# Performance work log

Measured on AMD Instinct MI355X. Metric: run time of the kernel, lower is better.

Reference implementation:

```python
import jax, jax.numpy as jnp
import numpy as np
import math

# Config (matches init_kwargs / input_specs)
N_ENT = 50000      # number of entities
N_REL = 500        # number of relations
HID = 64           # args.hidden_dim = per-axis dim d; entity dim = 3d, relation dim = 4d
E = 500000         # number of edges
EMB_RANGE = 1.0    # embedding_range
PI = 3.1415926235897933


def setup_inputs() -> dict:
    key = jax.random.key(0)
    k1, k2, k3, k4, k5 = jax.random.split(key, 5)
    entities = jax.random.normal(k1, (N_ENT, 3 * HID), dtype=jnp.float32)
    relations = jax.random.normal(k2, (N_REL, 4 * HID), dtype=jnp.float32)
    head = jax.random.randint(k3, (E,), 0, N_ENT, dtype=jnp.int32)
    rel = jax.random.randint(k4, (E,), 0, N_REL, dtype=jnp.int32)
    tail = jax.random.randint(k5, (E,), 0, N_ENT, dtype=jnp.int32)
    edge_index = jnp.stack([head, rel, tail], axis=0)  # (3, E)
    return {"entities": entities, "relations": relations, "edge_index": edge_index}


def do_trans(ent, rel):
    """Rot3DE rotation: rotate 3D entity point (per feature dim) by the
    quaternion encoded in rel = (axis_x, axis_y, axis_z, theta). is_head_rel=True branch.
    ent: (E, 3d), rel: (E, 4d) -> (E, 4d)"""
    ex, ey, ez = jnp.split(ent, 3, axis=-1)            # each (E, d)
    rx, ry, rz, theta = jnp.split(rel, 4, axis=-1)     # each (E, d)
    theta = theta / (EMB_RANGE / PI)
    sin = jnp.sin(theta)
    w = jnp.cos(theta)
    # F.normalize(stack([sin*rx, sin*ry, sin*rz]), dim=0): unit rotation axis (sign of sin folded in)
    t = jnp.stack([sin * rx, sin * ry, sin * rz], axis=0)  # (3, E, d)
    norm = jnp.sqrt(jnp.sum(t * t, axis=0, keepdims=True))
    n = t / jnp.maximum(norm, 1e-12)
    # quaternion q = (w, u) with u = |sin(theta)| * unit_axis  (sin sign already in n)
    s = jnp.sqrt(jnp.clip(1.0 - w * w, 0.0, None))
    ux, uy, uz = s * n[0], s * n[1], s * n[2]
    # Hamilton product q (x) p with pure quaternion p = (0, ex, ey, ez)  [head direction]
    x_score = w * ex + (uy * ez - uz * ey)
    y_score = w * ey + (uz * ex - ux * ez)
    z_score = w * ez + (ux * ey - uy * ex)
    w_score = -(ux * ex + uy * ey + uz * ez)
    return jnp.concatenate([x_score, y_score, z_score, w_score], axis=-1)  # (E, 4d)


def reference(entities, relations, edge_index):
    head, rel_id, tail = edge_index[0], edge_index[1], edge_index[2]
    # eff_do_trans's unique-based dedup is a pure compute optimization; the
    # math is identical to the direct per-edge transform below.
    qv = do_trans(entities[head], relations[rel_id])  # (E, 4d) keys/values
    # GAT_update: key = [gathered tail entity (3d) ; zeros(d)]
    k = jnp.concatenate(
        [entities[tail], jnp.zeros((E, HID), dtype=entities.dtype)], axis=-1
    )  # (E, 4d)
    embed_dim = 4 * HID
    alpha = jnp.sum(k * qv, axis=-1) / math.sqrt(embed_dim)  # (E,)
    # scatter_softmax over destination nodes (stable segment softmax)
    m = jax.ops.segment_max(alpha, tail, num_segments=N_ENT)
    m = jnp.where(jnp.isfinite(m), m, 0.0)  # empty segments
    e = jnp.exp(alpha - m[tail])
    denom = jax.ops.segment_sum(e, tail, num_segments=N_ENT)
    attn = e / denom[tail]  # (E,)
    # weighted scatter_add -> (N_ENT, 4d)
    out = jax.ops.segment_sum(qv * attn[:, None], tail, num_segments=N_ENT)
    return out
```

## Files before the change

### kernel.cpp

```cpp
#include <hip/hip_runtime.h>
#include <stdint.h>
#include <math.h>

#define HID 64
#define PI_F 3.14159262235897933f

__global__ void prep(const float* __restrict__ rel, float4* __restrict__ quat, int nrel,
                     const int* __restrict__ eidx, int E, int* __restrict__ hist,
                     int qblocks) {
    if ((int)blockIdx.x < qblocks) {
        int i = blockIdx.x * blockDim.x + threadIdx.x;
        if (i >= nrel * HID) return;
        int r = i >> 6, j = i & 63;
        const float* base = rel + (size_t)r * 4 * HID;
        float rx = base[j];
        float ry = base[HID + j];
        float rz = base[2 * HID + j];
        float th = base[3 * HID + j];
        float theta = th * PI_F;
        float sn = sinf(theta);
        float w  = cosf(theta);
        float tx = sn * rx, ty = sn * ry, tz = sn * rz;
        float norm = sqrtf(tx * tx + ty * ty + tz * tz);
        float inv = 1.0f / fmaxf(norm, 1e-12f);
        float s = sqrtf(fmaxf(1.0f - w * w, 0.0f));
        quat[i] = make_float4(w, s * tx * inv, s * ty * inv, s * tz * inv);
    } else {
        int e = (blockIdx.x - qblocks) * blockDim.x + threadIdx.x;
        if (e >= E) return;
        atomicAdd(hist + eidx[2 * E + e], 1);
    }
}

__global__ void scan1(const int* __restrict__ hist, int* __restrict__ base,
                      int* __restrict__ partial, int n) {
    __shared__ int buf[256];
    int tid = threadIdx.x;
    int gid = blockIdx.x * 256 + tid;
    int v = (gid < n) ? hist[gid] : 0;
    buf[tid] = v;
    __syncthreads();
    #pragma unroll
    for (int off = 1; off < 256; off <<= 1) {
        int x = (tid >= off) ? buf[tid - off] : 0;
        __syncthreads();
        buf[tid] += x;
        __syncthreads();
    }
    if (gid < n) base[gid] = buf[tid] - v;
    if (tid == 255) partial[blockIdx.x] = buf[255];
}

__global__ void scan23(int* __restrict__ base, int* __restrict__ base2,
                       const int* __restrict__ partial,
                       int nb, int n, int E) {
    __shared__ int buf[256];
    int tid = threadIdx.x;
    int v = (tid < nb) ? partial[tid] : 0;
    buf[tid] = v;
    __syncthreads();
    #pragma unroll
    for (int off = 1; off < 256; off <<= 1) {
        int x = (tid >= off) ? buf[tid - off] : 0;
        __syncthreads();
        buf[tid] += x;
        __syncthreads();
    }
    int bsum = ((int)blockIdx.x < nb) ? partial[blockIdx.x] : 0;
    int boff = buf[blockIdx.x] - bsum;
    int gid = blockIdx.x * 256 + tid;
    if (gid < n) {
        int bv = base[gid] + boff;
        base[gid] = bv;
        base2[gid] = bv;
    } else if (gid == n) {
        base[n] = E;
    }
}

__global__ void scatter_hr(const int* __restrict__ eidx, int E,
                           int* __restrict__ base2,
                           int2* __restrict__ hr) {
    int e = blockIdx.x * blockDim.x + threadIdx.x;
    if (e >= E) return;
    int t = eidx[2 * E + e];
    int pos = atomicAdd(base2 + t, 1);
    hr[pos] = make_int2(eidx[e], eidx[E + e]);
}

__global__ void seg_reduce(const float* __restrict__ ent,
                           const float4* __restrict__ quat,
                           const int2* __restrict__ hr,
                           const int* __restrict__ base,
                           int n_ent,
                           float* __restrict__ out) {
    const int lane = threadIdx.x & 63;
    const int sub = lane >> 4;
    const int j   = lane & 15;
    const int wid = (blockIdx.x * blockDim.x + threadIdx.x) >> 6;
    const int nw  = (gridDim.x * blockDim.x) >> 6;

    for (int t = wid; t < n_ent; t += nw) {
        int start = base[t];
        int end   = base[t + 1];
        float4* o4 = (float4*)(out + (size_t)t * (4 * HID));
        if (start == end) {
            o4[lane] = make_float4(0.f, 0.f, 0.f, 0.f);
            continue;
        }
        int last = end - 1;

        const float4* krow = (const float4*)(ent + (size_t)t * (3 * HID));
        float4 kx = krow[j], ky = krow[16 + j], kz = krow[32 + j];

        float dnm = 0.0f;
        float4 ax = make_float4(0.f, 0.f, 0.f, 0.f);
        float4 ay = ax, az = ax, aw = ax;

        for (int k0 = start; k0 < end; k0 += 4) {
            int e = k0 + sub;
            bool valid = (e < end);
            int2 her = hr[min(e, last)];
            const float4* h = (const float4*)(ent + (size_t)her.x * (3 * HID));
            float4 hx = h[j], hy = h[16 + j], hz = h[32 + j];
            const float4* qr = quat + (size_t)her.y * HID + 4 * j;
            float4 q0 = qr[0], q1 = qr[1], q2 = qr[2], q3 = qr[3];

            float4 qx, qy, qz, qw;
            float p = 0.0f;
            #define DO_DIM(F, Q) { \
                float ex = hx.F, ey = hy.F, ez = hz.F; \
                float w = Q.x, ux = Q.y, uy = Q.z, uz = Q.w; \
                float rqx = w * ex + uy * ez - uz * ey; \
                float rqy = w * ey + uz * ex - ux * ez; \
                float rqz = w * ez + ux * ey - uy * ex; \
                float rqw = -(ux * ex + uy * ey + uz * ez); \
                p += kx.F * rqx + ky.F * rqy + kz.F * rqz; \
                qx.F = rqx; qy.F = rqy; qz.F = rqz; qw.F = rqw; }
            DO_DIM(x, q0)
            DO_DIM(y, q1)
            DO_DIM(z, q2)
            DO_DIM(w, q3)
            #undef DO_DIM

            p += __shfl_xor(p, 1, 64);
            p += __shfl_xor(p, 2, 64);
            p += __shfl_xor(p, 4, 64);
            p += __shfl_xor(p, 8, 64);

            float pe = valid ? __expf(p * 0.0625f) : 0.0f;
            dnm += pe;
            ax.x += pe * qx.x; ax.y += pe * qx.y; ax.z += pe * qx.z; ax.w += pe * qx.w;
            ay.x += pe * qy.x; ay.y += pe * qy.y; ay.z += pe * qy.z; ay.w += pe * qy.w;
            az.x += pe * qz.x; az.y += pe * qz.y; az.z += pe * qz.z; az.w += pe * qz.w;
            aw.x += pe * qw.x; aw.y += pe * qw.y; aw.z += pe * qw.z; aw.w += pe * qw.w;
        }

        #pragma unroll
        for (int mask = 16; mask <= 32; mask <<= 1) {
            dnm += __shfl_xor(dnm, mask, 64);
            ax.x += __shfl_xor(ax.x, mask, 64); ax.y += __shfl_xor(ax.y, mask, 64);
            ax.z += __shfl_xor(ax.z, mask, 64); ax.w += __shfl_xor(ax.w, mask, 64);
            ay.x += __shfl_xor(ay.x, mask, 64); ay.y += __shfl_xor(ay.y, mask, 64);
            ay.z += __shfl_xor(ay.z, mask, 64); ay.w += __shfl_xor(ay.w, mask, 64);
            az.x += __shfl_xor(az.x, mask, 64); az.y += __shfl_xor(az.y, mask, 64);
            az.z += __shfl_xor(az.z, mask, 64); az.w += __shfl_xor(az.w, mask, 64);
            aw.x += __shfl_xor(aw.x, mask, 64); aw.y += __shfl_xor(aw.y, mask, 64);
            aw.z += __shfl_xor(aw.z, mask, 64); aw.w += __shfl_xor(aw.w, mask, 64);
        }

        float inv = (dnm > 0.0f) ? 1.0f / dnm : 0.0f;
        float4 lo = (sub & 1) ? ay : ax;
        float4 hi = (sub & 1) ? aw : az;
        float4 val = (sub & 2) ? hi : lo;
        val.x *= inv; val.y *= inv; val.z *= inv; val.w *= inv;
        o4[lane] = val;
    }
}

extern "C" void kernel_launch(void* const* d_in, const int* in_sizes, int n_in,
                              void* d_out, int out_size, void* d_ws, size_t ws_size,
                              hipStream_t stream) {
    const float* ent  = (const float*)d_in[0];
    const float* rel  = (const float*)d_in[1];
    const int*   eidx = (const int*)d_in[2];
    float* out = (float*)d_out;

    const int n_ent = in_sizes[0] / (3 * HID);
    const int n_rel = in_sizes[1] / (4 * HID);
    const int E     = in_sizes[2] / 3;

    int2* hr     = (int2*)d_ws;
    int*  hist   = (int*)(hr + E);
    int*  base   = hist + n_ent;
    int*  base2  = base + n_ent + 1;
    int*  partial= base2 + n_ent;
    uintptr_t p = (uintptr_t)(partial + 256);
    p = (p + 15) & ~(uintptr_t)15;
    float4* quat = (float4*)p;

    hipMemsetAsync(hist, 0, (size_t)n_ent * sizeof(int), stream);

    const int qblocks  = (n_rel * HID + 255) / 256;
    const int eblocks1 = (E + 255) / 256;
    prep<<<qblocks + eblocks1, 256, 0, stream>>>(rel, quat, n_rel, eidx, E, hist, qblocks);

    const int nb = (n_ent + 255) / 256;
    scan1<<<nb, 256, 0, stream>>>(hist, base, partial, n_ent);
    scan23<<<(n_ent + 1 + 255) / 256, 256, 0, stream>>>(base, base2, partial, nb, n_ent, E);

    scatter_hr<<<eblocks1, 256, 0, stream>>>(eidx, E, base2, hr);

    seg_reduce<<<2048, 256, 0, stream>>>(ent, quat, hr, base, n_ent, out);
}
```

Baseline: 146.3 us.

## Split each destination segment across two wavefronts with shared-memory combine

The segment reduction now assigns two wavefronts to each destination entity, each taking interleaved groups of four edges. The partial accumulators and denominators are merged through shared memory after a block barrier. This replaces the grid-stride loop of one wavefront per entity with one block per two entities, aiming to shorten the per-segment serial dependency chain and raise memory-level parallelism. In exchange it adds a barrier, shared-memory traffic, and a much larger grid with fixed per-block overhead.

```diff
diff --git a/kernel.cpp b/kernel.cpp
--- a/kernel.cpp
+++ b/kernel.cpp
@@ -88,36 +88,36 @@
     hr[pos] = make_int2(eidx[e], eidx[E + e]);
 }
 
-__global__ void seg_reduce(const float* __restrict__ ent,
-                           const float4* __restrict__ quat,
-                           const int2* __restrict__ hr,
-                           const int* __restrict__ base,
-                           int n_ent,
-                           float* __restrict__ out) {
+__global__ void __launch_bounds__(256)
+seg_reduce(const float* __restrict__ ent,
+           const float4* __restrict__ quat,
+           const int2* __restrict__ hr,
+           const int* __restrict__ base,
+           int n_ent,
+           float* __restrict__ out) {
+    __shared__ float4 part[2][64];
+    __shared__ float pdnm[2];
     const int lane = threadIdx.x & 63;
-    const int sub = lane >> 4;
-    const int j   = lane & 15;
-    const int wid = (blockIdx.x * blockDim.x + threadIdx.x) >> 6;
-    const int nw  = (gridDim.x * blockDim.x) >> 6;
-
-    for (int t = wid; t < n_ent; t += nw) {
-        int start = base[t];
-        int end   = base[t + 1];
-        float4* o4 = (float4*)(out + (size_t)t * (4 * HID));
-        if (start == end) {
-            o4[lane] = make_float4(0.f, 0.f, 0.f, 0.f);
-            continue;
-        }
+    const int wv   = threadIdx.x >> 6;
+    const int pair = wv >> 1;
+    const int q    = wv & 1;
+    const int sub  = lane >> 4;
+    const int j    = lane & 15;
+    const int t    = blockIdx.x * 2 + pair;
+
+    float dnm = 0.0f;
+    float4 ax = make_float4(0.f, 0.f, 0.f, 0.f);
+    float4 ay = ax, az = ax, aw = ax;
+
+    int start = 0, end = 0;
+    if (t < n_ent) { start = base[t]; end = base[t + 1]; }
+
+    if (start < end) {
         int last = end - 1;
-
         const float4* krow = (const float4*)(ent + (size_t)t * (3 * HID));
         float4 kx = krow[j], ky = krow[16 + j], kz = krow[32 + j];
 
-        float dnm = 0.0f;
-        float4 ax = make_float4(0.f, 0.f, 0.f, 0.f);
-        float4 ay = ax, az = ax, aw = ax;
-
-        for (int k0 = start; k0 < end; k0 += 4) {
+        for (int k0 = start + 4 * q; k0 < end; k0 += 8) {
             int e = k0 + sub;
             bool valid = (e < end);
             int2 her = hr[min(e, last)];
@@ -168,12 +168,24 @@
             aw.x += __shfl_xor(aw.x, mask, 64); aw.y += __shfl_xor(aw.y, mask, 64);
             aw.z += __shfl_xor(aw.z, mask, 64); aw.w += __shfl_xor(aw.w, mask, 64);
         }
-
-        float inv = (dnm > 0.0f) ? 1.0f / dnm : 0.0f;
-        float4 lo = (sub & 1) ? ay : ax;
-        float4 hi = (sub & 1) ? aw : az;
-        float4 val = (sub & 2) ? hi : lo;
+    }
+
+    float4 lo = (sub & 1) ? ay : ax;
+    float4 hi = (sub & 1) ? aw : az;
+    float4 val = (sub & 2) ? hi : lo;
+
+    if (q == 1) {
+        part[pair][lane] = val;
+        if (lane == 0) pdnm[pair] = dnm;
+    }
+    __syncthreads();
+    if (q == 0 && t < n_ent) {
+        float4 v1 = part[pair][lane];
+        float dtot = dnm + pdnm[pair];
+        val.x += v1.x; val.y += v1.y; val.z += v1.z; val.w += v1.w;
+        float inv = (dtot > 0.0f) ? 1.0f / dtot : 0.0f;
         val.x *= inv; val.y *= inv; val.z *= inv; val.w *= inv;
+        float4* o4 = (float4*)(out + (size_t)t * (4 * HID));
         o4[lane] = val;
     }
 }
@@ -211,5 +223,6 @@
 
     scatter_hr<<<eblocks1, 256, 0, stream>>>(eidx, E, base2, hr);
 
-    seg_reduce<<<2048, 256, 0, stream>>>(ent, quat, hr, base, n_ent, out);
-}
+    const int sblocks = (n_ent + 1) / 2;
+    seg_reduce<<<sblocks, 256, 0, stream>>>(ent, quat, hr, base, n_ent, out);
+}
```

After: 152.0 us. 1.04x slower.
